# Performance work log

Measured on AMD Instinct MI355X. Metric: run time of the kernel, lower is better.

Reference implementation:

```python
import jax, jax.numpy as jnp
import numpy as np

B, CD, ZL = 512, 64, 16
HID, SE, NC, SL = 512, 512, 9, 64
EPS = 1e-5


def _conv_t1d(x, w, b, stride, opad):
    # torch ConvTranspose1d weight layout: [in, out, k]; pad=0
    k = w.shape[-1]
    w2 = jnp.flip(jnp.transpose(w, (1, 0, 2)), -1)  # [out, in, k]
    y = jax.lax.conv_general_dilated(
        x, w2, window_strides=(1,),
        padding=[(k - 1, k - 1 + opad)], lhs_dilation=(stride,),
        dimension_numbers=('NCH', 'OIH', 'NCH'))
    return y + b[None, :, None]


def _bn(x, g, bt, m, v):  # eval-mode BatchNorm1d over channel dim of [B,C,L]
    return (x - m[None, :, None]) * (g * jax.lax.rsqrt(v + EPS))[None, :, None] + bt[None, :, None]


def _gru(x, h, wih, whh, bih, bhh):  # torch GRUCell gate order r,z,n
    gi = x @ wih.T + bih
    gh = h @ whh.T + bhh
    ir, iz, inn = jnp.split(gi, 3, axis=-1)
    hr, hz, hn = jnp.split(gh, 3, axis=-1)
    r = jax.nn.sigmoid(ir + hr)
    z = jax.nn.sigmoid(iz + hz)
    n = jnp.tanh(inn + r * hn)
    return (1.0 - z) * n + z * h


def setup_inputs() -> dict:
    ks = jax.random.split(jax.random.key(0), 24)
    s = 0.05
    H2 = HID // 2
    in1 = H2 + 2 * NC
    d = {}
    d['quantized_z'] = jax.random.normal(ks[0], (B, CD, ZL), jnp.float32)
    d['note_target'] = (jax.random.uniform(ks[1], (B, SL, NC)) > 0.5).astype(jnp.float32)
    d['skel'] = (jax.random.uniform(ks[2], (B, SL, NC)) > 0.5).astype(jnp.float32)
    d['skel_encoded'] = jax.random.normal(ks[3], (B, SE), jnp.float32)
    d['training'] = 0
    d['teacher_forcing_ratio'] = 0
    d['ct1_w'] = jax.random.normal(ks[4], (CD, HID, 4)) * s
    d['ct1_b'] = jnp.zeros((HID,))
    d['bn1_g'] = jnp.ones((HID,))
    d['bn1_b'] = jnp.zeros((HID,))
    d['bn1_m'] = jax.random.normal(ks[5], (HID,)) * 0.1
    d['bn1_v'] = 1.0 + 0.1 * jax.random.uniform(ks[6], (HID,))
    d['ct2_w'] = jax.random.normal(ks[7], (HID, H2, 4)) * s
    d['ct2_b'] = jnp.zeros((H2,))
    d['bn2_g'] = jnp.ones((H2,))
    d['bn2_b'] = jnp.zeros((H2,))
    d['bn2_m'] = jax.random.normal(ks[8], (H2,)) * 0.1
    d['bn2_v'] = 1.0 + 0.1 * jax.random.uniform(ks[9], (H2,))
    d['hfc_w'] = jax.random.normal(ks[10], (HID, SE)) * s
    d['hfc_b'] = jnp.zeros((HID,))
    d['gru1_wih'] = jax.random.normal(ks[11], (3 * HID, in1)) * s
    d['gru1_whh'] = jax.random.normal(ks[12], (3 * HID, HID)) * s
    d['gru1_bih'] = jnp.zeros((3 * HID,))
    d['gru1_bhh'] = jnp.zeros((3 * HID,))
    d['gru2_wih'] = jax.random.normal(ks[13], (3 * HID, HID)) * s
    d['gru2_whh'] = jax.random.normal(ks[14], (3 * HID, HID)) * s
    d['gru2_bih'] = jnp.zeros((3 * HID,))
    d['gru2_bhh'] = jnp.zeros((3 * HID,))
    d['nfc_w'] = jax.random.normal(ks[15], (NC, HID)) * s
    d['nfc_b'] = jnp.zeros((NC,))
    return d


def _forward(quantized_z, skel, skel_encoded,
             ct1_w, ct1_b, bn1_g, bn1_b, bn1_m, bn1_v,
             ct2_w, ct2_b, bn2_g, bn2_b, bn2_m, bn2_v,
             hfc_w, hfc_b,
             gru1_wih, gru1_whh, gru1_bih, gru1_bhh,
             gru2_wih, gru2_whh, gru2_bih, gru2_bhh,
             nfc_w, nfc_b):
    lrelu = lambda x: jax.nn.leaky_relu(x, 0.2)
    y = lrelu(_bn(_conv_t1d(quantized_z, ct1_w, ct1_b, 2, 1), bn1_g, bn1_b, bn1_m, bn1_v))
    y = lrelu(_bn(_conv_t1d(y, ct2_w, ct2_b, 2, 0), bn2_g, bn2_b, bn2_m, bn2_v))
    inputs = jnp.transpose(y, (0, 2, 1))[:, :SL]  # [B, SL, HID//2]
    h1_0 = skel_encoded @ hfc_w.T + hfc_b          # [B, HID]
    keys = jax.random.split(jax.random.key(42), SL)

    def step(carry, xs):
        h1, h2, out = carry
        i, x_in, x_sk, k = xs
        cat = jnp.concatenate([out, x_in, x_sk], axis=-1)  # [B, NC + HID//2 + NC]
        h1 = _gru(cat, h1, gru1_wih, gru1_whh, gru1_bih, gru1_bhh)
        h2 = jnp.where(i == 0, h1, h2)  # hx[1] = hx[0] at first step
        h2 = _gru(h1, h2, gru2_wih, gru2_whh, gru2_bih, gru2_bhh)
        logits = h2 @ nfc_w.T + nfc_b
        r = jax.random.uniform(k, logits.shape, logits.dtype)
        out = (jax.nn.sigmoid(logits) - r > 0).astype(logits.dtype)  # eval-mode Bernoulli sampling
        return (h1, h2, out), logits

    carry0 = (h1_0, jnp.zeros_like(h1_0), jnp.zeros((quantized_z.shape[0], NC), h1_0.dtype))
    xs = (jnp.arange(SL), jnp.transpose(inputs, (1, 0, 2)), jnp.transpose(skel, (1, 0, 2)), keys)
    _, logits = jax.lax.scan(step, carry0, xs)
    return jnp.transpose(logits, (1, 0, 2))  # [B, SL, NC]


def reference(quantized_z, note_target, skel, skel_encoded, training, teacher_forcing_ratio,
              ct1_w, ct1_b, bn1_g, bn1_b, bn1_m, bn1_v,
              ct2_w, ct2_b, bn2_g, bn2_b, bn2_m, bn2_v,
              hfc_w, hfc_b,
              gru1_wih, gru1_whh, gru1_bih, gru1_bhh,
              gru2_wih, gru2_whh, gru2_bih, gru2_bhh,
              nfc_w, nfc_b):
    # training=0 (eval): dropout is identity, BN uses running stats, always sample feedback.
    # note_target / teacher_forcing_ratio are unused on the eval path.
    return _forward(quantized_z, skel, skel_encoded,
                    ct1_w, ct1_b, bn1_g, bn1_b, bn1_m, bn1_v,
                    ct2_w, ct2_b, bn2_g, bn2_b, bn2_m, bn2_v,
                    hfc_w, hfc_b,
                    gru1_wih, gru1_whh, gru1_bih, gru1_bhh,
                    gru2_wih, gru2_whh, gru2_bih, gru2_bhh,
                    nfc_w, nfc_b)
```

## Files before the change

kernel.cpp:

```cpp
#include <hip/hip_runtime.h>
#include <stdint.h>

typedef uint32_t u32; typedef uint16_t u16; typedef unsigned long long u64;
typedef __attribute__((ext_vector_type(8))) short short8;
typedef __attribute__((ext_vector_type(4))) float f32x4;

#define DEV static __device__ __forceinline__
#define MFMA16 __builtin_amdgcn_mfma_f32_16x16x32_bf16

#define BATCH 512
#define CD    64
#define ZL    16
#define HID   512
#define H2D   256
#define NC    9
#define SLEN  64
#define L1    35

#define JAX_PARTITIONABLE 1

#define P_W      2850816
#define WOFF_SKH 4276224
#define WOFF_HPL 4538368
#define WOFF_HF  6111232
#define WOFF_LOG 7159808
#define WOFF_FLG 7684096
#define WOFF_XH  9175040

template<int V> struct IC { static constexpr int value = V; };

DEV float bf2f(u16 h){ u32 u = ((u32)h) << 16; float f; __builtin_memcpy(&f,&u,4); return f; }
DEV u16 f2bf(float f){ u32 u; __builtin_memcpy(&u,&f,4); return (u16)((u + 0x7FFFu + ((u>>16)&1u)) >> 16); }

DEV float ldf(const float* p){ return __hip_atomic_load(p, __ATOMIC_RELAXED, __HIP_MEMORY_SCOPE_AGENT); }
DEV u32 ldu32(const u32* p){ return __hip_atomic_load(p, __ATOMIC_RELAXED, __HIP_MEMORY_SCOPE_AGENT); }
DEV u64 ldu64(const u64* p){ return __hip_atomic_load(p, __ATOMIC_RELAXED, __HIP_MEMORY_SCOPE_AGENT); }
DEV void stu32(u32* p, u32 v){ __hip_atomic_store(p, v, __ATOMIC_RELAXED, __HIP_MEMORY_SCOPE_AGENT); }

DEV void threefry2x32(u32 k0, u32 k1, u32 x0, u32 x1, u32 &o0, u32 &o1){
  const u32 ks2 = k0 ^ k1 ^ 0x1BD11BDAu;
#define TF_R(d) { x0 += x1; x1 = (x1 << (d)) | (x1 >> (32 - (d))); x1 ^= x0; }
  x0 += k0; x1 += k1;
  TF_R(13) TF_R(15) TF_R(26) TF_R(6)
  x0 += k1;  x1 += ks2 + 1u;
  TF_R(17) TF_R(29) TF_R(16) TF_R(24)
  x0 += ks2; x1 += k0 + 2u;
  TF_R(13) TF_R(15) TF_R(26) TF_R(6)
  x0 += k0;  x1 += k1 + 3u;
  TF_R(17) TF_R(29) TF_R(16) TF_R(24)
  x0 += k1;  x1 += ks2 + 4u;
  TF_R(13) TF_R(15) TF_R(26) TF_R(6)
  x0 += ks2; x1 += k0 + 5u;
#undef TF_R
  o0 = x0; o1 = x1;
}
DEV void step_key(int t, u32 &ka, u32 &kb){
#if JAX_PARTITIONABLE
  threefry2x32(0u, 42u, 0u, (u32)t, ka, kb);
#else
  u32 j0 = 2u*(u32)t, j1 = j0 + 1u, a0, a1;
  if (j0 < 64u){ threefry2x32(0u,42u, j0, 64u+j0, a0, a1); ka = a0; }
  else         { threefry2x32(0u,42u, j0-64u, j0, a0, a1); ka = a1; }
  if (j1 < 64u){ threefry2x32(0u,42u, j1, 64u+j1, a0, a1); kb = a0; }
  else         { threefry2x32(0u,42u, j1-64u, j1, a0, a1); kb = a1; }
#endif
}
DEV float rng_uniform(u32 ka, u32 kb, u32 f){
  u32 bits, o0, o1;
#if JAX_PARTITIONABLE
  threefry2x32(ka, kb, 0u, f, o0, o1);
  bits = o0 ^ o1;
#else
  const u32 HALF = (u32)(BATCH*NC/2);
  if (f < HALF){ threefry2x32(ka, kb, f, f+HALF, o0, o1); bits = o0; }
  else         { threefry2x32(ka, kb, f-HALF, f, o0, o1); bits = o1; }
#endif
  u32 fb = (bits >> 9) | 0x3F800000u;
  float fv; __builtin_memcpy(&fv,&fb,4);
  return fv - 1.0f;
}

__global__ __launch_bounds__(256) void k_conv1(
    const float* __restrict__ z, const float* __restrict__ w1, const float* __restrict__ b1,
    const float* __restrict__ g1, const float* __restrict__ bt1, const float* __restrict__ m1,
    const float* __restrict__ v1, float* __restrict__ y1out)
{
  int t = blockIdx.x, bg = blockIdx.y*8, tid = threadIdx.x;
  __shared__ float zsh[2][8][CD];
  int k0 = t & 1, sA = (t-k0)>>1, sB = sA-1;
  bool vA = (sA>=0 && sA<ZL), vB = (sB>=0 && sB<ZL);
  for (int l = tid; l < 2*8*CD; l += 256){
    int p = l>>9, bb = (l>>6)&7, i = l&63;
    int s = p ? sB : sA; bool v = p ? vB : vA;
    zsh[p][bb][i] = v ? z[((bg+bb)*CD+i)*ZL + s] : 0.f;
  }
  __syncthreads();
  const float4* w1v = (const float4*)w1;
  for (int o = tid; o < HID; o += 256){
    float acc[8] = {0,0,0,0,0,0,0,0};
    for (int i = 0; i < CD; i++){
      float4 wv = w1v[i*HID + o];
      float wA = k0 ? wv.y : wv.x, wB = k0 ? wv.w : wv.z;
      #pragma unroll
      for (int bb = 0; bb < 8; bb++) acc[bb] += zsh[0][bb][i]*wA + zsh[1][bb][i]*wB;
    }
    float xb = b1[o], sc = g1[o]/sqrtf(v1[o]+1e-5f), mm = m1[o], be = bt1[o];
    #pragma unroll
    for (int bb = 0; bb < 8; bb++){
      float y = (acc[bb]+xb-mm)*sc + be;
      y = (y>0.f)? y : 0.2f*y;
      y1out[((bg+bb)*L1 + t)*HID + o] = y;
    }
  }
}

__global__ __launch_bounds__(256) void k_conv2(
    const float* __restrict__ y1, const float* __restrict__ w2, const float* __restrict__ b2,
    const float* __restrict__ g2, const float* __restrict__ bt2, const float* __restrict__ m2,
    const float* __restrict__ v2, u16* __restrict__ xh, u16* __restrict__ xl)
{
  int t = blockIdx.x, bg = blockIdx.y*8, tid = threadIdx.x;
  __shared__ float ysh[2][8][HID];
  int k0 = t & 1, sA = (t-k0)>>1, sB = sA-1;
  bool vB = (sB >= 0);
  for (int l = tid; l < 2*8*HID; l += 256){
    int p = l>>12, bb = (l>>9)&7, o = l&511;
    int s = p ? sB : sA; bool v = p ? vB : true;
    ysh[p][bb][o] = v ? y1[((bg+bb)*L1 + s)*HID + o] : 0.f;
  }
  __syncthreads();
  int c = tid;
  float acc[8] = {0,0,0,0,0,0,0,0};
  const float4* w2v = (const float4*)w2;
  for (int o4 = 0; o4 < HID; o4 += 4){
    float wA[4], wB[4];
    #pragma unroll
    for (int j = 0; j < 4; j++){
      float4 wv = w2v[(o4+j)*H2D + c];
      wA[j] = k0 ? wv.y : wv.x; wB[j] = k0 ? wv.w : wv.z;
    }
    #pragma unroll
    for (int bb = 0; bb < 8; bb++){
      const float4 ya = *(const float4*)&ysh[0][bb][o4];
      const float4 yb = *(const float4*)&ysh[1][bb][o4];
      acc[bb] += ya.x*wA[0]+ya.y*wA[1]+ya.z*wA[2]+ya.w*wA[3]
               + yb.x*wB[0]+yb.y*wB[1]+yb.z*wB[2]+yb.w*wB[3];
    }
  }
  float xb = b2[c], sc = g2[c]/sqrtf(v2[c]+1e-5f), mm = m2[c], be = bt2[c];
  #pragma unroll
  for (int bb = 0; bb < 8; bb++){
    float y = (acc[bb]+xb-mm)*sc + be;
    y = (y>0.f)? y : 0.2f*y;
    u16 hi = f2bf(y); u16 lo = f2bf(y - bf2f(hi));
    size_t o = ((size_t)t*512 + bg + bb)*256 + c;
    xh[o] = hi; xl[o] = lo;
  }
}

__global__ __launch_bounds__(256) void k_prep(
    const float* __restrict__ wih1, const float* __restrict__ whh1,
    const float* __restrict__ wih2, const float* __restrict__ whh2,
    const float* __restrict__ skel, float* __restrict__ ws)
{
  u16* wp = (u16*)ws;
  u16* skh = (u16*)(ws + WOFF_SKH);
  float* logacc = ws + WOFF_LOG;
  u32* flg = (u32*)(ws + WOFF_FLG);
  int stride = gridDim.x*256, i0 = blockIdx.x*256 + threadIdx.x;
  for (int i = i0; i < P_W; i += stride){
    int r = i; float v;
    if (r < 491520){
      int n = r/320, k = r - n*320; v = 0.f;
      if (k < 256)      v = wih1[(size_t)n*274 + 9 + k];
      else if (k < 265) v = wih1[(size_t)n*274 + 265 + (k-256)];
      else if (k < 274) v = wih1[(size_t)n*274 + (k-265)];
    }
    else if (r < 1277952){ int rr = r-491520;  int n = rr>>9, k = rr&511; v = whh1[((size_t)n<<9)+k]; }
    else if (r < 2064384){ int rr = r-1277952; int n = rr>>9, k = rr&511; v = wih2[((size_t)n<<9)+k]; }
    else                 { int rr = r-2064384; int n = rr>>9, k = rr&511; v = whh2[((size_t)n<<9)+k]; }
    u16 l0 = f2bf(v);
    float r1 = v - bf2f(l0); u16 l1 = f2bf(r1);
    float r2 = r1 - bf2f(l1); u16 l2 = f2bf(r2);
    wp[i] = l0; wp[P_W + i] = l1; wp[2*P_W + i] = l2;
  }
  for (int i = i0; i < 524288; i += stride){
    int c = i & 15, r = i >> 4, b = r & 511, tt = r >> 9;
    float v = (c < 9) ? skel[((size_t)b*64 + tt)*9 + c] : 0.f;
    skh[i] = f2bf(v);
  }
  for (int i = i0; i < 524288; i += stride) logacc[i] = 0.f;
  for (int i = i0; i < 512; i += stride) flg[i] = 0u;
}

__global__ __launch_bounds__(256) void k_h0(
    const float* __restrict__ se, const float* __restrict__ w, const float* __restrict__ bias,
    float* __restrict__ ws)
{
  float* h1af = ws + WOFF_HF;
  u16* hpl = (u16*)(ws + WOFF_HPL);
  int b = blockIdx.x, tid = threadIdx.x;
  __shared__ float ssh[HID];
  for (int i = tid; i < HID; i += 256) ssh[i] = se[b*HID + i];
  __syncthreads();
  for (int j = tid; j < HID; j += 256){
    float acc = 0.f;
    for (int q = 0; q < HID; q++) acc += ssh[q]*w[j*HID + q];
    float v = acc + bias[j];
    h1af[(size_t)b*512 + j] = v;
    u16 l0 = f2bf(v);
    float r1 = v - bf2f(l0); u16 l1 = f2bf(r1);
    float r2 = r1 - bf2f(l1); u16 l2 = f2bf(r2);
    hpl[(size_t)b*512 + j] = l0;
    hpl[262144 + (size_t)b*512 + j] = l1;
    hpl[524288 + (size_t)b*512 + j] = l2;
  }
}

__global__ __launch_bounds__(768, 1) void k_persist(
    float* __restrict__ ws,
    const float* __restrict__ bih1, const float* __restrict__ bhh1,
    const float* __restrict__ bih2, const float* __restrict__ bhh2,
    const float* __restrict__ nfw,  const float* __restrict__ nfb,
    float* __restrict__ dout)
{
  const int tid = threadIdx.x;
  const int wvid = __builtin_amdgcn_readfirstlane(tid >> 6);
  const int g  = wvid >> 2;
  const int mh = (wvid >> 1) & 1;
  const int jn = wvid & 1;
  const int lane = tid & 63;
  const int mloc = lane & 15;
  const int q8 = (lane >> 4) * 8;
  const int q4 = (lane >> 4) * 4;
  const int bid = blockIdx.x;
  const int xcd = bid & 7;
  const int rr2 = bid >> 3;
  const int bg = rr2 >> 1;
  const int nstrip = (xcd << 1) | (rr2 & 1);
  const int b0 = bg * 32;
  const int n0 = nstrip * 32;

  u16* wp = (u16*)ws;
  const u16* skh = (const u16*)(ws + WOFF_SKH);
  u16* hpl = (u16*)(ws + WOFF_HPL);
  const float* h1af = ws + WOFF_HF;
  float* logacc = ws + WOFF_LOG;
  u32* flgH = (u32*)(ws + WOFF_FLG);
  u32* flgL = flgH + 256;
  const u16* xh = (const u16*)(ws + WOFF_XH);
  const u16* xl = xh + 8388608;

  __shared__ __align__(16) u16 Abuf[2][3][32][72];
  __shared__ __align__(16) u16 Wbuf[2][3][3][32][72];
  __shared__ __align__(16) float eg[4][32][33];
  __shared__ __align__(16) float h2loc[32][33];
  __shared__ __align__(16) u16 out_sh[32][12];

  int t = 0;
  float2 hp1 = {0.f,0.f}, hp2 = {0.f,0.f};

  if (tid < 384) ((u16*)out_sh)[tid] = 0;
  if (tid < 512){
    int bi = tid >> 4, nl2 = (tid & 15)*2;
    hp1.x = h1af[(size_t)(b0+bi)*512 + n0 + nl2];
    hp1.y = h1af[(size_t)(b0+bi)*512 + n0 + nl2 + 1];
  }

  auto soft_bar = [&](){
    __builtin_amdgcn_sched_barrier(0);
    asm volatile("s_waitcnt lgkmcnt(0)" ::: "memory");
    __builtin_amdgcn_s_barrier();
    __builtin_amdgcn_sched_barrier(0);
  };
  auto arrive = [&](u32* f, u32 tok){
    __syncthreads();
    if (tid == 0) __hip_atomic_store(&f[bg*16 + nstrip], tok, __ATOMIC_RELEASE, __HIP_MEMORY_SCOPE_AGENT);
  };
  auto waitbar = [&](u32* f, u32 tok){
    if (tid < 16) while (ldu32(&f[bg*16 + tid]) < tok) __builtin_amdgcn_s_sleep(2);
    __syncthreads();
  };

  auto run_phase = [&](auto mc, auto nwc, int Kp, size_t SUB, const u16* hb, f32x4 &acc){
    constexpr int MODE = decltype(mc)::value;
    constexpr int NW = decltype(nwc)::value;
    short8 RwA[3], RwB[3];
    u64 RaA[2], RaB[2];

    auto loadW = [&](short8 (&R)[3], int kc){
      #pragma unroll
      for (int i = 0; i < 3; i++){
        int idx = tid + i*768;
        int gp = idx >> 8, r = idx & 255, nn = r >> 3, ck = r & 7;
        const u16* src = wp + (size_t)(gp % 3)*P_W + SUB
                       + ((size_t)((gp/3)*512 + n0 + nn))*(size_t)Kp + kc + ck*8;
        R[i] = *(const short8*)src;
      }
    };
    auto writeW = [&](int buf, short8 (&R)[3]){
      #pragma unroll
      for (int i = 0; i < 3; i++){
        int idx = tid + i*768;
        int gp = idx >> 8, r = idx & 255, nn = r >> 3, ck = r & 7;
        *(short8*)&Wbuf[buf][gp/3][gp%3][nn][ck*8] = R[i];
      }
    };
    auto loadA = [&](u64 (&R)[2], int kc){
      int idx = tid;
      if constexpr (MODE == 1){
        int p = idx >> 8, r = idx & 255, bi = r >> 3, ck = r & 7;
        const u16* src = hb + (size_t)p*262144 + (size_t)(b0+bi)*512 + kc + ck*8;
        R[0] = ldu64((const u64*)src);
        R[1] = ldu64((const u64*)(src + 4));
      } else {
        if (idx < 512){
          int p = idx >> 8, r = idx & 255, bi = r >> 3, ck = r & 7;
          if (kc < 256){
            const u64* src = (const u64*)((p ? xl : xh) + ((size_t)t*512 + b0 + bi)*256 + kc + ck*8);
            R[0] = src[0]; R[1] = src[1];
          } else {
            u64 w0 = 0, w1 = 0;
            if (p == 0){
              #pragma unroll
              for (int e2 = 0; e2 < 4; e2++){
                int kg = 256 + ck*8 + e2;
                u16 val = 0;
                if (kg < 265) val = skh[((size_t)t*512 + b0 + bi)*16 + (kg - 256)];
                else if (kg < 274) val = out_sh[bi][kg - 265];
                w0 |= ((u64)val) << (16*e2);
              }
              #pragma unroll
              for (int e2 = 0; e2 < 4; e2++){
                int kg = 260 + ck*8 + e2;
                u16 val = 0;
                if (kg < 265) val = skh[((size_t)t*512 + b0 + bi)*16 + (kg - 256)];
                else if (kg < 274) val = out_sh[bi][kg - 265];
                w1 |= ((u64)val) << (16*e2);
              }
            }
            R[0] = w0; R[1] = w1;
          }
        }
      }
    };
    auto writeA = [&](int buf, u64 (&R)[2]){
      constexpr int NCH = (MODE == 1) ? 768 : 512;
      int idx = tid;
      if (idx < NCH){
        int p = idx >> 8, r = idx & 255, bi = r >> 3, ck = r & 7;
        u64* d = (u64*)&Abuf[buf][p][bi][ck*8];
        d[0] = R[0]; d[1] = R[1];
      }
    };
    auto compute = [&](int buf){
      const int ar = mh*16 + mloc;
      const int wr = jn*16 + mloc;
      #pragma unroll
      for (int ks = 0; ks < 2; ks++){
        const int ko = ks*32 + q8;
        short8 a0 = *(const short8*)&Abuf[buf][0][ar][ko];
        short8 a1 = *(const short8*)&Abuf[buf][1][ar][ko];
        short8 a2 = {};
        if constexpr (MODE == 1) a2 = *(const short8*)&Abuf[buf][2][ar][ko];
        short8 w0 = *(const short8*)&Wbuf[buf][g][0][wr][ko];
        short8 w1 = *(const short8*)&Wbuf[buf][g][1][wr][ko];
        short8 w2 = *(const short8*)&Wbuf[buf][g][2][wr][ko];
        acc = MFMA16(a0, w0, acc, 0, 0, 0);
        acc = MFMA16(a0, w1, acc, 0, 0, 0);
        acc = MFMA16(a1, w0, acc, 0, 0, 0);
        acc = MFMA16(a0, w2, acc, 0, 0, 0);
        if constexpr (MODE == 1) acc = MFMA16(a2, w0, acc, 0, 0, 0);
        acc = MFMA16(a1, w1, acc, 0, 0, 0);
      }
    };

    loadW(RwA, 0); loadA(RaA, 0);
    loadW(RwB, 64); loadA(RaB, 64);
    writeW(0, RwA); writeA(0, RaA);
    soft_bar();

    auto stepw = [&](int w, short8 (&Rl)[3], u64 (&Al)[2], short8 (&Rs)[3], u64 (&As)[2]){
      if (w + 2 < NW){ loadW(Rl, (w+2)*64); loadA(Al, (w+2)*64); }
      compute(w & 1);
      if (w + 1 < NW){ writeW((w+1)&1, Rs); writeA((w+1)&1, As); }
      soft_bar();
    };
    #pragma unroll
    for (int w = 0; w < NW; w += 2){
      stepw(w, RwA, RaA, RwB, RaB);
      if (w + 1 < NW) stepw(w+1, RwB, RaB, RwA, RaA);
    }
  };

  auto epilogue = [&](const float* bih, const float* bhh, u16* hnl,
                      float2 &hp, bool cell2, bool init2,
                      const f32x4 &accI, const f32x4 &accH){
    #pragma unroll
    for (int i2 = 0; i2 < 4; i2++){
      int row = mh*16 + q4 + i2, col = jn*16 + mloc;
      if (g < 2) eg[g][row][col] = accI[i2] + accH[i2];
      else { eg[2][row][col] = accI[i2]; eg[3][row][col] = accH[i2]; }
    }
    __syncthreads();
    if (tid < 512){
      int bi = tid >> 4, nl2 = (tid & 15)*2, b = b0 + bi;
      float hv[2];
      float hpv0 = hp.x, hpv1 = hp.y;
      #pragma unroll
      for (int u = 0; u < 2; u++){
        int nl = nl2 + u, n = n0 + nl;
        float rr = 1.f/(1.f + expf(-(eg[0][bi][nl] + bih[n] + bhh[n])));
        float zz = 1.f/(1.f + expf(-(eg[1][bi][nl] + bih[512+n] + bhh[512+n])));
        float nn2 = tanhf(eg[2][bi][nl] + bih[1024+n] + rr*(eg[3][bi][nl] + bhh[1024+n]));
        float hprev = u ? hpv1 : hpv0;
        hv[u] = (1.f - zz)*nn2 + zz*hprev;
        if (cell2) h2loc[bi][nl] = hv[u];
      }
      hp.x = hv[0]; hp.y = hv[1];
      if (init2){ hp2.x = hv[0]; hp2.y = hv[1]; }
      u16 A0 = f2bf(hv[0]); float ra = hv[0] - bf2f(A0);
      u16 A1 = f2bf(ra);    float ra2 = ra - bf2f(A1);
      u16 A2 = f2bf(ra2);
      u16 B0 = f2bf(hv[1]); float rb = hv[1] - bf2f(B0);
      u16 B1 = f2bf(rb);    float rb2 = rb - bf2f(B1);
      u16 B2 = f2bf(rb2);
      size_t base = (size_t)b*512 + n0 + nl2;
      stu32((u32*)(hnl + base),          (u32)A0 | ((u32)B0 << 16));
      stu32((u32*)(hnl + 262144 + base), (u32)A1 | ((u32)B1 << 16));
      stu32((u32*)(hnl + 524288 + base), (u32)A2 | ((u32)B2 << 16));
    }
    __syncthreads();
    if (cell2){
      for (int e = tid; e < 288; e += 768){
        int c = e % 9, bi = e / 9;
        float s = 0.f;
        #pragma unroll
        for (int nl = 0; nl < 32; nl++) s += nfw[c*512 + n0 + nl]*h2loc[bi][nl];
        atomicAdd(&logacc[((size_t)t*512 + b0 + bi)*16 + c], s);
      }
    }
  };

  auto sample_phase = [&](int tp){
    for (int e = tid; e < 288; e += 768){
      int c = e % 9, bi = e / 9, b = b0 + bi;
      float lg = ldf(&logacc[((size_t)tp*512 + b)*16 + c]) + nfb[c];
      if (nstrip == 0) dout[((size_t)b*64 + tp)*9 + c] = lg;
      if (tp < 63){
        u32 ka, kb; step_key(tp, ka, kb);
        float rr = rng_uniform(ka, kb, (u32)(b*9 + c));
        float sg = 1.f/(1.f + expf(-lg));
        out_sh[bi][c] = (sg - rr > 0.f) ? (u16)0x3F80 : (u16)0;
      }
    }
    __syncthreads();
  };

  for (t = 0; t < 64; t++){
    const u16* h1pl = hpl + (size_t)((t & 1) ? 1 : 0)*786432;
    u16*       h1nl = hpl + (size_t)((t & 1) ? 0 : 1)*786432;
    const u16* h2pl = hpl + (size_t)((t & 1) ? 2 : 3)*786432;
    u16*       h2nl = hpl + (size_t)((t & 1) ? 3 : 2)*786432;

    f32x4 accI = {0,0,0,0}, accH = {0,0,0,0};
    run_phase(IC<1>{}, IC<8>{}, 512, (size_t)491520, h1pl, accH);
    if (t > 0){ waitbar(flgL, (u32)t); sample_phase(t-1); }
    run_phase(IC<0>{}, IC<5>{}, 320, (size_t)0, nullptr, accI);
    epilogue(bih1, bhh1, h1nl, hp1, false, (t == 0), accI, accH);
    arrive(flgH, (u32)(t+1));

    f32x4 accI2 = {0,0,0,0}, accH2 = {0,0,0,0};
    if (t == 0){
      waitbar(flgH, 1u);
      run_phase(IC<1>{}, IC<8>{}, 512, (size_t)2064384, h1nl, accH2);
    } else {
      run_phase(IC<1>{}, IC<8>{}, 512, (size_t)2064384, h2pl, accH2);
      waitbar(flgH, (u32)(t+1));
    }
    run_phase(IC<1>{}, IC<8>{}, 512, (size_t)1277952, h1nl, accI2);
    epilogue(bih2, bhh2, h2nl, hp2, true, false, accI2, accH2);
    arrive(flgL, (u32)(t+1));
  }
  waitbar(flgL, 64u);
  sample_phase(63);
}

extern "C" void kernel_launch(void* const* d_in, const int* in_sizes, int n_in,
                              void* d_out, int out_size, void* d_ws, size_t ws_size,
                              hipStream_t stream) {
  (void)in_sizes; (void)n_in; (void)out_size; (void)ws_size;
  const float* z       = (const float*)d_in[0];
  const float* skel    = (const float*)d_in[2];
  const float* se      = (const float*)d_in[3];
  const float* ct1_w   = (const float*)d_in[6];
  const float* ct1_b   = (const float*)d_in[7];
  const float* bn1_g   = (const float*)d_in[8];
  const float* bn1_b   = (const float*)d_in[9];
  const float* bn1_m   = (const float*)d_in[10];
  const float* bn1_v   = (const float*)d_in[11];
  const float* ct2_w   = (const float*)d_in[12];
  const float* ct2_b   = (const float*)d_in[13];
  const float* bn2_g   = (const float*)d_in[14];
  const float* bn2_b   = (const float*)d_in[15];
  const float* bn2_m   = (const float*)d_in[16];
  const float* bn2_v   = (const float*)d_in[17];
  const float* hfc_w   = (const float*)d_in[18];
  const float* hfc_b   = (const float*)d_in[19];
  const float* g1_wih  = (const float*)d_in[20];
  const float* g1_whh  = (const float*)d_in[21];
  const float* g1_bih  = (const float*)d_in[22];
  const float* g1_bhh  = (const float*)d_in[23];
  const float* g2_wih  = (const float*)d_in[24];
  const float* g2_whh  = (const float*)d_in[25];
  const float* g2_bih  = (const float*)d_in[26];
  const float* g2_bhh  = (const float*)d_in[27];
  const float* nfc_w   = (const float*)d_in[28];
  const float* nfc_b   = (const float*)d_in[29];

  float* ws = (float*)d_ws;
  float* y1 = ws;
  u16* xh = (u16*)(ws + WOFF_XH);
  u16* xl = xh + 8388608;
  float* dout = (float*)d_out;

  k_conv1<<<dim3(L1, BATCH/8), 256, 0, stream>>>(z, ct1_w, ct1_b, bn1_g, bn1_b, bn1_m, bn1_v, y1);
  k_conv2<<<dim3(SLEN, BATCH/8), 256, 0, stream>>>(y1, ct2_w, ct2_b, bn2_g, bn2_b, bn2_m, bn2_v, xh, xl);
  k_prep<<<4096, 256, 0, stream>>>(g1_wih, g1_whh, g2_wih, g2_whh, skel, ws);
  k_h0<<<BATCH, 256, 0, stream>>>(se, hfc_w, hfc_b, ws);

  void* args[] = {
    (void*)&ws, (void*)&g1_bih, (void*)&g1_bhh, (void*)&g2_bih, (void*)&g2_bhh,
    (void*)&nfc_w, (void*)&nfc_b, (void*)&dout
  };
  hipLaunchCooperativeKernel((const void*)k_persist, dim3(256), dim3(768), args, 0, stream);
}
```

Baseline: 3.608 ms.

## Load GRU weight fragments directly into registers instead of staging through LDS

Each wave now loads its own MFMA weight operands for all three limbs straight from global memory into registers, double-buffered across k-chunks, and the shared-memory weight buffer with its write step is removed. This drops the LDS write/read round trip for weights and frees a large LDS allocation, which may allow higher occupancy. In exchange it uses more vector registers, and the global loads are less coalesced because each lane fetches 16-byte pieces from separate rows. The next weight load is now issued after the compute for the current chunk.

```diff
diff --git a/kernel.cpp b/kernel.cpp
--- a/kernel.cpp
+++ b/kernel.cpp
@@ -252,7 +252,6 @@
   const u16* xl = xh + 8388608;
 
   __shared__ __align__(16) u16 Abuf[2][3][32][72];
-  __shared__ __align__(16) u16 Wbuf[2][3][3][32][72];
   __shared__ __align__(16) float eg[4][32][33];
   __shared__ __align__(16) float h2loc[32][33];
   __shared__ __align__(16) u16 out_sh[32][12];
@@ -285,26 +284,17 @@
   auto run_phase = [&](auto mc, auto nwc, int Kp, size_t SUB, const u16* hb, f32x4 &acc){
     constexpr int MODE = decltype(mc)::value;
     constexpr int NW = decltype(nwc)::value;
-    short8 RwA[3], RwB[3];
+    short8 RWA[6], RWB[6];
     u64 RaA[2], RaB[2];
 
-    auto loadW = [&](short8 (&R)[3], int kc){
+    const u16* wbase = wp + SUB + (size_t)(g*512 + n0 + jn*16 + mloc)*(size_t)Kp + q8;
+
+    auto loadW = [&](short8 (&R)[6], int kc){
       #pragma unroll
-      for (int i = 0; i < 3; i++){
-        int idx = tid + i*768;
-        int gp = idx >> 8, r = idx & 255, nn = r >> 3, ck = r & 7;
-        const u16* src = wp + (size_t)(gp % 3)*P_W + SUB
-                       + ((size_t)((gp/3)*512 + n0 + nn))*(size_t)Kp + kc + ck*8;
-        R[i] = *(const short8*)src;
-      }
-    };
-    auto writeW = [&](int buf, short8 (&R)[3]){
-      #pragma unroll
-      for (int i = 0; i < 3; i++){
-        int idx = tid + i*768;
-        int gp = idx >> 8, r = idx & 255, nn = r >> 3, ck = r & 7;
-        *(short8*)&Wbuf[buf][gp/3][gp%3][nn][ck*8] = R[i];
-      }
+      for (int limb = 0; limb < 3; limb++)
+        #pragma unroll
+        for (int ks = 0; ks < 2; ks++)
+          R[limb*2 + ks] = *(const short8*)(wbase + (size_t)limb*P_W + kc + ks*32);
     };
     auto loadA = [&](u64 (&R)[2], int kc){
       int idx = tid;
@@ -353,9 +343,8 @@
         d[0] = R[0]; d[1] = R[1];
       }
     };
-    auto compute = [&](int buf){
+    auto compute = [&](int buf, short8 (&RW)[6]){
       const int ar = mh*16 + mloc;
-      const int wr = jn*16 + mloc;
       #pragma unroll
       for (int ks = 0; ks < 2; ks++){
         const int ko = ks*32 + q8;
@@ -363,9 +352,9 @@
         short8 a1 = *(const short8*)&Abuf[buf][1][ar][ko];
         short8 a2 = {};
         if constexpr (MODE == 1) a2 = *(const short8*)&Abuf[buf][2][ar][ko];
-        short8 w0 = *(const short8*)&Wbuf[buf][g][0][wr][ko];
-        short8 w1 = *(const short8*)&Wbuf[buf][g][1][wr][ko];
-        short8 w2 = *(const short8*)&Wbuf[buf][g][2][wr][ko];
+        short8 w0 = RW[0*2 + ks];
+        short8 w1 = RW[1*2 + ks];
+        short8 w2 = RW[2*2 + ks];
         acc = MFMA16(a0, w0, acc, 0, 0, 0);
         acc = MFMA16(a0, w1, acc, 0, 0, 0);
         acc = MFMA16(a1, w0, acc, 0, 0, 0);
@@ -375,21 +364,22 @@
       }
     };
 
-    loadW(RwA, 0); loadA(RaA, 0);
-    loadW(RwB, 64); loadA(RaB, 64);
-    writeW(0, RwA); writeA(0, RaA);
+    loadW(RWA, 0); loadA(RaA, 0);
+    loadW(RWB, 64); loadA(RaB, 64);
+    writeA(0, RaA);
     soft_bar();
 
-    auto stepw = [&](int w, short8 (&Rl)[3], u64 (&Al)[2], short8 (&Rs)[3], u64 (&As)[2]){
-      if (w + 2 < NW){ loadW(Rl, (w+2)*64); loadA(Al, (w+2)*64); }
-      compute(w & 1);
-      if (w + 1 < NW){ writeW((w+1)&1, Rs); writeA((w+1)&1, As); }
+    auto stepw = [&](int w, short8 (&RWc)[6], u64 (&Al)[2], u64 (&As)[2]){
+      if (w + 2 < NW) loadA(Al, (w+2)*64);
+      compute(w & 1, RWc);
+      if (w + 2 < NW) loadW(RWc, (w+2)*64);
+      if (w + 1 < NW) writeA((w+1)&1, As);
       soft_bar();
     };
     #pragma unroll
     for (int w = 0; w < NW; w += 2){
-      stepw(w, RwA, RaA, RwB, RaB);
-      if (w + 1 < NW) stepw(w+1, RwB, RaB, RwA, RaA);
+      stepw(w, RWA, RaA, RaB);
+      if (w + 1 < NW) stepw(w+1, RWB, RaB, RaA);
     }
   };
 
```

Result: slower. 7.495 ms (+107.7%).
